# Kernel optimization log

Hardware: AMD Instinct MI355X
Metric: run time of the kernel (lower is better)

The kernel has to match this reference:

```python
import jax, jax.numpy as jnp
import numpy as np

OBS_LEN = 8
PRED_LEN = 12
BATCH = 65536
EMB = 64
H = 64


def setup_inputs() -> dict:
    key = jax.random.key(0)
    ks = jax.random.split(key, 18)
    s = 1.0 / np.sqrt(H)  # torch default uniform bound scale, used as std here

    def p(k, shape):
        return (jax.random.normal(k, shape, dtype=jnp.float32) * s).astype(jnp.float32)

    return {
        "obs_traj": jax.random.normal(ks[0], (OBS_LEN, BATCH, 2), dtype=jnp.float32),
        "obs_traj_rel": jax.random.normal(ks[1], (OBS_LEN, BATCH, 2), dtype=jnp.float32),
        # encoder params
        "enc_emb_w": p(ks[2], (EMB, 2)),
        "enc_emb_b": p(ks[3], (EMB,)),
        "enc_w_ih": p(ks[4], (4 * H, EMB)),
        "enc_w_hh": p(ks[5], (4 * H, H)),
        "enc_b_ih": p(ks[6], (4 * H,)),
        "enc_b_hh": p(ks[7], (4 * H,)),
        # decoder params
        "dec_emb_w": p(ks[8], (EMB, 2)),
        "dec_emb_b": p(ks[9], (EMB,)),
        "dec_w_ih": p(ks[10], (4 * H, EMB)),
        "dec_w_hh": p(ks[11], (4 * H, H)),
        "dec_b_ih": p(ks[12], (4 * H,)),
        "dec_b_hh": p(ks[13], (4 * H,)),
        "h2p_w": p(ks[14], (2, H)),
        "h2p_b": p(ks[15], (2,)),
    }


def _lstm_cell(h, c, x, w_ih, w_hh, b_ih, b_hh):
    # torch nn.LSTM gate order: i, f, g, o
    gates = x @ w_ih.T + h @ w_hh.T + (b_ih + b_hh)
    i, f, g, o = jnp.split(gates, 4, axis=-1)
    c_new = jax.nn.sigmoid(f) * c + jax.nn.sigmoid(i) * jnp.tanh(g)
    h_new = jax.nn.sigmoid(o) * jnp.tanh(c_new)
    return h_new, c_new


def reference(obs_traj, obs_traj_rel,
              enc_emb_w, enc_emb_b, enc_w_ih, enc_w_hh, enc_b_ih, enc_b_hh,
              dec_emb_w, dec_emb_b, dec_w_ih, dec_w_hh, dec_b_ih, dec_b_hh,
              h2p_w, h2p_b):
    batch = obs_traj_rel.shape[1]

    # ---------- Encoder ----------
    enc_in = obs_traj_rel @ enc_emb_w.T + enc_emb_b  # [T, B, EMB]

    def enc_step(carry, x_t):
        h, c = carry
        h, c = _lstm_cell(h, c, x_t, enc_w_ih, enc_w_hh, enc_b_ih, enc_b_hh)
        return (h, c), None

    h0 = jnp.zeros((batch, H), dtype=obs_traj_rel.dtype)
    c0 = jnp.zeros((batch, H), dtype=obs_traj_rel.dtype)
    (h_enc, _), _ = jax.lax.scan(enc_step, (h0, c0), enc_in)

    # ---------- Decoder ----------
    dec_h = h_enc                                   # final encoder hidden seeds decoder
    dec_c = jnp.zeros((batch, H), dtype=obs_traj_rel.dtype)
    last_pos_rel = obs_traj_rel[-1]
    dec_in = last_pos_rel @ dec_emb_w.T + dec_emb_b  # [B, EMB]

    def dec_step(carry, _):
        h, c, x = carry
        h, c = _lstm_cell(h, c, x, dec_w_ih, dec_w_hh, dec_b_ih, dec_b_hh)
        rel_pos = h @ h2p_w.T + h2p_b               # [B, 2]
        x_next = rel_pos @ dec_emb_w.T + dec_emb_b  # [B, EMB]
        return (h, c, x_next), rel_pos

    (_, _, _), pred_traj_fake_rel = jax.lax.scan(
        dec_step, (dec_h, dec_c, dec_in), None, length=PRED_LEN)
    return pred_traj_fake_rel  # [PRED_LEN, B, 2]
```

## Files before the change

kernel.cpp:

```cpp
#include <hip/hip_runtime.h>

#define OBS_LEN 8
#define PRED_LEN 12
#define TILE_B 32
#define NTHREADS 256

typedef __attribute__((ext_vector_type(8))) short short8;
typedef __attribute__((ext_vector_type(4))) float floatx4;
typedef __attribute__((ext_vector_type(2))) float floatx2;
typedef __attribute__((ext_vector_type(2))) unsigned int u32x2;
typedef unsigned short u16;
typedef unsigned int u32;

#define L2E 1.442695040888963f

__device__ __forceinline__ u16 f2bf(float f) {
  __bf16 b = (__bf16)f;
  return __builtin_bit_cast(u16, b);
}
__device__ __forceinline__ float bf2f(u16 h) {
  return __builtin_bit_cast(float, ((u32)h) << 16);
}
__device__ __forceinline__ float rndbf(float f) { return (float)(__bf16)f; }

#if __has_builtin(__builtin_amdgcn_exp2f)
__device__ __forceinline__ float fexp2_(float x) { return __builtin_amdgcn_exp2f(x); }
#else
__device__ __forceinline__ float fexp2_(float x) { return exp2f(x); }
#endif
__device__ __forceinline__ floatx2 exp2v(floatx2 x) {
  floatx2 r;
  r.x = fexp2_(x.x);
  r.y = fexp2_(x.y);
  return r;
}
#if __has_builtin(__builtin_amdgcn_rcpf)
__device__ __forceinline__ floatx2 rcp2(floatx2 x) {
  floatx2 r;
  r.x = __builtin_amdgcn_rcpf(x.x);
  r.y = __builtin_amdgcn_rcpf(x.y);
  return r;
}
#else
__device__ __forceinline__ floatx2 rcp2(floatx2 x) {
  return floatx2{1.0f / x.x, 1.0f / x.y};
}
#endif

__device__ __forceinline__ floatx4 mfma_bf(short8 a, short8 b, floatx4 c) {
  return __builtin_amdgcn_mfma_f32_16x16x32_bf16(a, b, c, 0, 0, 0);
}

__device__ __forceinline__ int swz(int s, int b) {
  return s * 64 + ((b ^ (s & 7)) * 8);
}

__device__ __forceinline__ void load_afrags(const float* __restrict__ W,
                                            short8 (&af)[4][2],
                                            int u0, int q, int l16) {
#pragma unroll
  for (int t = 0; t < 4; ++t)
#pragma unroll
    for (int kf = 0; kf < 2; ++kf) {
      const float* src = W + (t * 64 + u0 + l16) * 64 + kf * 32 + q * 8;
      const floatx4 w0 = *(const floatx4*)src;
      const floatx4 w1 = *(const floatx4*)(src + 4);
      short8 a;
#pragma unroll
      for (int j = 0; j < 4; ++j) {
        a[j] = (short)f2bf(w0[j]);
        a[j + 4] = (short)f2bf(w1[j]);
      }
      af[t][kf] = a;
    }
}

__device__ __forceinline__ void load_afrags_eff(const float* __restrict__ Whh,
                                                const float* __restrict__ aS0,
                                                const float* __restrict__ aS1,
                                                const float* __restrict__ hw0,
                                                const float* __restrict__ hw1,
                                                short8 (&af)[4][2],
                                                int u0, int q, int l16) {
#pragma unroll
  for (int t = 0; t < 4; ++t) {
    const int g = t * 64 + u0 + l16;
    const float a0 = aS0[g], a1 = aS1[g];
#pragma unroll
    for (int kf = 0; kf < 2; ++kf) {
      const int u = kf * 32 + q * 8;
      const float* src = Whh + g * 64 + u;
      const floatx4 w0 = *(const floatx4*)src;
      const floatx4 w1 = *(const floatx4*)(src + 4);
      const floatx4 p00 = *(const floatx4*)(hw0 + u);
      const floatx4 p01 = *(const floatx4*)(hw0 + u + 4);
      const floatx4 p10 = *(const floatx4*)(hw1 + u);
      const floatx4 p11 = *(const floatx4*)(hw1 + u + 4);
      short8 a;
#pragma unroll
      for (int j = 0; j < 4; ++j) {
        a[j] = (short)f2bf(w0[j] + a0 * p00[j] + a1 * p10[j]);
        a[j + 4] = (short)f2bf(w1[j] + a0 * p01[j] + a1 * p11[j]);
      }
      af[t][kf] = a;
    }
  }
}

__device__ __forceinline__ void nonlin_store(const floatx4 (&acc)[4],
                                             floatx2 (&c2)[2],
                                             u16* __restrict__ wrh,
                                             int s, int q, int wv) {
  const int sw = s & 7;
  u32 hpk[2];
#pragma unroll
  for (int p = 0; p < 2; ++p) {
    const floatx2 iv = {acc[0][2 * p], acc[0][2 * p + 1]};
    const floatx2 fv = {acc[1][2 * p], acc[1][2 * p + 1]};
    const floatx2 gv = {acc[2][2 * p], acc[2][2 * p + 1]};
    const floatx2 ov = {acc[3][2 * p], acc[3][2 * p + 1]};
    const floatx2 ei = exp2v(iv * -L2E);
    const floatx2 ef = exp2v(fv * -L2E);
    const floatx2 eg = exp2v(gv * (2.0f * L2E));
    const floatx2 eo = exp2v(ov * -L2E);
    const floatx2 A = ei + 1.0f;
    const floatx2 F = ef + 1.0f;
    const floatx2 Bg = eg + 1.0f;
    const floatx2 P = A * Bg;
    const floatx2 num = c2[p] * P + (eg - 1.0f) * F;
    const floatx2 cn = num * rcp2(F * P);
    c2[p] = cn;
    const floatx2 ec = exp2v(cn * (2.0f * L2E));
    const floatx2 h = (ec - 1.0f) * rcp2((eo + 1.0f) * (ec + 1.0f));
    hpk[p] = (u32)f2bf(h.x) | ((u32)f2bf(h.y) << 16);
  }
  *(u32x2*)(wrh + s * 64 + (((wv * 2 + (q >> 1)) ^ sw) * 8) + (q & 1) * 4) =
      u32x2{hpk[0], hpk[1]};
}

__device__ __forceinline__ void cell_step(const u16* __restrict__ rdh,
                                          const u16* __restrict__ rdx,
                                          u16* __restrict__ wrh,
                                          const short8 (&afh)[4][2],
                                          const short8 (&afx)[4][2],
                                          const float* __restrict__ biasrow,
                                          floatx2 (&c)[2][2],
                                          int q, int l16, int wv, int u0) {
#pragma unroll
  for (int n = 0; n < 2; ++n) {
    const int s = n * 16 + l16;
    const int sw = s & 7;
    const u16* hr = rdh + s * 64;
    const u16* xr = rdx + s * 64;
    const short8 hb0 = *(const short8*)(hr + ((q ^ sw) * 8));
    const short8 hb1 = *(const short8*)(hr + (((q + 4) ^ sw) * 8));
    const short8 xb0 = *(const short8*)(xr + ((q ^ sw) * 8));
    const short8 xb1 = *(const short8*)(xr + (((q + 4) ^ sw) * 8));
    floatx4 acc[4];
#pragma unroll
    for (int t = 0; t < 4; ++t) {
      const floatx4 bias = *(const floatx4*)(biasrow + t * 64 + u0 + q * 4);
      acc[t] = mfma_bf(afh[t][0], hb0, bias);
    }
#pragma unroll
    for (int t = 0; t < 4; ++t) acc[t] = mfma_bf(afx[t][0], xb0, acc[t]);
#pragma unroll
    for (int t = 0; t < 4; ++t) acc[t] = mfma_bf(afh[t][1], hb1, acc[t]);
#pragma unroll
    for (int t = 0; t < 4; ++t) acc[t] = mfma_bf(afx[t][1], xb1, acc[t]);
    nonlin_store(acc, c[n], wrh, s, q, wv);
  }
}

__device__ __forceinline__ void dec_step_folded(
    const u16* __restrict__ rdh, u16* __restrict__ wrh,
    const short8 (&af)[4][2], const short8 (&afp)[2],
    const float* __restrict__ biasrow, float b2p0, float b2p1,
    float* __restrict__ relrow,
    floatx2 (&c)[2][2], int q, int l16, int wv, int u0) {
  short8 hb0[2], hb1[2];
#pragma unroll
  for (int n = 0; n < 2; ++n) {
    const int s = n * 16 + l16, sw = s & 7;
    const u16* hr = rdh + s * 64;
    hb0[n] = *(const short8*)(hr + ((q ^ sw) * 8));
    hb1[n] = *(const short8*)(hr + (((q + 4) ^ sw) * 8));
  }
  floatx4 acc[2][4];
#pragma unroll
  for (int t = 0; t < 4; ++t) {
    const floatx4 bias = *(const floatx4*)(biasrow + t * 64 + u0 + q * 4);
    acc[0][t] = mfma_bf(af[t][0], hb0[0], bias);
    acc[1][t] = mfma_bf(af[t][0], hb0[1], bias);
  }
#pragma unroll
  for (int t = 0; t < 4; ++t) {
    acc[0][t] = mfma_bf(af[t][1], hb1[0], acc[0][t]);
    acc[1][t] = mfma_bf(af[t][1], hb1[1], acc[1][t]);
  }
  if (wv < 2) {
    const short8 ha = wv ? hb0[1] : hb0[0];
    const short8 hc = wv ? hb1[1] : hb1[0];
    floatx4 ar = mfma_bf(afp[0], ha, floatx4{0.f, 0.f, 0.f, 0.f});
    ar = mfma_bf(afp[1], hc, ar);
    if (q == 0)
      *(floatx2*)(relrow + (wv * 16 + l16) * 2) =
          floatx2{ar[0] + b2p0, ar[1] + b2p1};
  }
#pragma unroll
  for (int n = 0; n < 2; ++n)
    nonlin_store(acc[n], c[n], wrh, n * 16 + l16, q, wv);
}

__device__ __forceinline__ void xgen8(float rb0, float rb1,
                                      const float* __restrict__ ew0,
                                      const float* __restrict__ ew1,
                                      const float* __restrict__ eb,
                                      u16* __restrict__ xw, int s8, int p8) {
  short8 v;
#pragma unroll
  for (int j = 0; j < 8; ++j) {
    const int e = p8 * 8 + j;
    v[j] = (short)f2bf(rb0 * ew0[e] + (rb1 * ew1[e] + eb[e]));
  }
  *(short8*)(xw + swz(s8, p8)) = v;
}

__global__ void __launch_bounds__(NTHREADS, 3)
lstm_kernel(const float* __restrict__ obs_rel,
            const float* __restrict__ enc_emb_w, const float* __restrict__ enc_emb_b,
            const float* __restrict__ enc_w_ih, const float* __restrict__ enc_w_hh,
            const float* __restrict__ enc_b_ih, const float* __restrict__ enc_b_hh,
            const float* __restrict__ dec_emb_w, const float* __restrict__ dec_emb_b,
            const float* __restrict__ dec_w_ih, const float* __restrict__ dec_w_hh,
            const float* __restrict__ dec_b_ih, const float* __restrict__ dec_b_hh,
            const float* __restrict__ h2p_w, const float* __restrict__ h2p_b,
            float* __restrict__ out, int batch) {
  __shared__ __align__(16) u16 hS[2][TILE_B * 64];
  __shared__ __align__(16) u16 xS[2][TILE_B * 64];
  __shared__ __align__(16) float posS[OBS_LEN][TILE_B * 2];
  __shared__ __align__(16) float biasS[3][256];
  __shared__ float ew0e[64], ew1e[64], ebe[64];
  __shared__ float ew0d[64], ew1d[64], ebd[64];
  __shared__ __align__(16) float aS0[256], aS1[256];
  __shared__ __align__(16) float hw0S[64], hw1S[64];
  __shared__ __align__(16) float relS[PRED_LEN][TILE_B * 2];

  const int tid = threadIdx.x;
  const int wv = tid >> 6, lane = tid & 63;
  const int q = lane >> 4, l16 = lane & 15;
  const int u0 = wv << 4;
  const int s8 = tid >> 3, p8 = tid & 7;
  const long S0 = (long)blockIdx.x * TILE_B;

  if (tid < 128) {
    const int t = tid >> 4, i = tid & 15;
    *(floatx4*)&posS[t][i * 4] =
        *(const floatx4*)(obs_rel + (long)t * batch * 2 + S0 * 2 + i * 4);
  }
  if (tid < 64) {
    ew0e[tid] = rndbf(enc_emb_w[tid * 2]);
    ew1e[tid] = rndbf(enc_emb_w[tid * 2 + 1]);
    ebe[tid] = enc_emb_b[tid];
    ew0d[tid] = rndbf(dec_emb_w[tid * 2]);
    ew1d[tid] = rndbf(dec_emb_w[tid * 2 + 1]);
    ebd[tid] = dec_emb_b[tid];
    hw0S[tid] = h2p_w[tid];
    hw1S[tid] = h2p_w[64 + tid];
  }
  biasS[0][tid] = enc_b_ih[tid] + enc_b_hh[tid];
  {
    float A0 = 0.f, A1 = 0.f, B0 = 0.f;
    const float* wr = dec_w_ih + tid * 64;
#pragma unroll
    for (int e4 = 0; e4 < 16; ++e4) {
      const floatx4 w = *(const floatx4*)(wr + e4 * 4);
      const floatx4 m0 = *(const floatx4*)(dec_emb_w + e4 * 8);
      const floatx4 m1 = *(const floatx4*)(dec_emb_w + e4 * 8 + 4);
      const floatx4 bb = *(const floatx4*)(dec_emb_b + e4 * 4);
      A0 += w[0] * m0[0] + w[1] * m0[2] + w[2] * m1[0] + w[3] * m1[2];
      A1 += w[0] * m0[1] + w[1] * m0[3] + w[2] * m1[1] + w[3] * m1[3];
      B0 += w[0] * bb[0] + w[1] * bb[1] + w[2] * bb[2] + w[3] * bb[3];
    }
    aS0[tid] = A0;
    aS1[tid] = A1;
    const float db = dec_b_ih[tid] + dec_b_hh[tid];
    biasS[1][tid] = db;
    biasS[2][tid] = db + B0 + A0 * h2p_b[0] + A1 * h2p_b[1];
  }
  for (int i = tid; i < TILE_B * 64 / 2; i += NTHREADS) ((u32*)&hS[0][0])[i] = 0;

  short8 afh[4][2], afx[4][2];
  floatx2 c[2][2];
  load_afrags(enc_w_hh, afh, u0, q, l16);
  load_afrags(enc_w_ih, afx, u0, q, l16);
  c[0][0] = c[0][1] = c[1][0] = c[1][1] = floatx2{0.f, 0.f};
  const float b2p0 = h2p_b[0], b2p1 = h2p_b[1];
  __syncthreads();
  {
    const floatx2 rr = *(const floatx2*)(&posS[0][s8 * 2]);
    xgen8(rndbf(rr.x), rndbf(rr.y), ew0e, ew1e, ebe, xS[0], s8, p8);
  }
  __syncthreads();

  int pb = 0;
#pragma unroll 1
  for (int t = 0; t < OBS_LEN; ++t) {
    const int tn = t + 1;
    const floatx2 rr = *(const floatx2*)(&posS[(tn < 8) ? tn : 7][s8 * 2]);
    if (tn < 8)
      xgen8(rndbf(rr.x), rndbf(rr.y), ew0e, ew1e, ebe, xS[tn & 1], s8, p8);
    else
      xgen8(rndbf(rr.x), rndbf(rr.y), ew0d, ew1d, ebd, xS[0], s8, p8);
    cell_step(hS[pb], xS[t & 1], hS[pb ^ 1], afh, afx, &biasS[0][0], c,
              q, l16, wv, u0);
    __syncthreads();
    pb ^= 1;
  }

  load_afrags(dec_w_hh, afh, u0, q, l16);
  load_afrags(dec_w_ih, afx, u0, q, l16);
  c[0][0] = c[0][1] = c[1][0] = c[1][1] = floatx2{0.f, 0.f};
  cell_step(hS[pb], xS[0], hS[pb ^ 1], afh, afx, &biasS[1][0], c,
            q, l16, wv, u0);
  load_afrags_eff(dec_w_hh, aS0, aS1, hw0S, hw1S, afh, u0, q, l16);
  short8 afp[2];
#pragma unroll
  for (int kf = 0; kf < 2; ++kf) {
    const int kb = kf * 32 + q * 8;
    short8 a;
#pragma unroll
    for (int j = 0; j < 4; ++j) {
      const float r0 = (l16 == 0) ? hw0S[kb + j] : (l16 == 1) ? hw1S[kb + j] : 0.f;
      const float r1 =
          (l16 == 0) ? hw0S[kb + 4 + j] : (l16 == 1) ? hw1S[kb + 4 + j] : 0.f;
      a[j] = (short)f2bf(r0);
      a[j + 4] = (short)f2bf(r1);
    }
    afp[kf] = a;
  }
  __syncthreads();
  pb ^= 1;

#pragma unroll 1
  for (int j = 1; j < PRED_LEN; ++j) {
    dec_step_folded(hS[pb], hS[pb ^ 1], afh, afp, &biasS[2][0], b2p0, b2p1,
                    &relS[j - 1][0], c, q, l16, wv, u0);
    __syncthreads();
    pb ^= 1;
  }

  if (wv < 2) {
    const int s = wv * 16 + l16, sw = s & 7;
    const u16* hr = hS[pb] + s * 64;
    const short8 ha = *(const short8*)(hr + ((q ^ sw) * 8));
    const short8 hc = *(const short8*)(hr + (((q + 4) ^ sw) * 8));
    floatx4 ar = mfma_bf(afp[0], ha, floatx4{0.f, 0.f, 0.f, 0.f});
    ar = mfma_bf(afp[1], hc, ar);
    if (q == 0)
      *(floatx2*)(&relS[PRED_LEN - 1][s * 2]) =
          floatx2{ar[0] + b2p0, ar[1] + b2p1};
  }
  __syncthreads();

#pragma unroll
  for (int r = 0; r < 3; ++r) {
    const int f = tid + r * 256;
    const int j = f >> 6, e = f & 63;
    out[(long)j * batch * 2 + S0 * 2 + e] = ((const float*)relS)[f];
  }
}

extern "C" void kernel_launch(void* const* d_in, const int* in_sizes, int n_in,
                              void* d_out, int out_size, void* d_ws, size_t ws_size,
                              hipStream_t stream) {
  const float* obs_rel = (const float*)d_in[1];
  const int batch = in_sizes[1] / (OBS_LEN * 2);

  const int blocks = batch / TILE_B;
  hipLaunchKernelGGL(lstm_kernel, dim3(blocks), dim3(NTHREADS), 0, stream,
                     obs_rel,
                     (const float*)d_in[2], (const float*)d_in[3],
                     (const float*)d_in[4], (const float*)d_in[5],
                     (const float*)d_in[6], (const float*)d_in[7],
                     (const float*)d_in[8], (const float*)d_in[9],
                     (const float*)d_in[10], (const float*)d_in[11],
                     (const float*)d_in[12], (const float*)d_in[13],
                     (const float*)d_in[14], (const float*)d_in[15],
                     (float*)d_out, batch);
}
```

Baseline: 218.5 us.

## Fold encoder input embedding into rank-2 gate weights, drop x tiles

Folds the embedding linear layer into the input-to-hidden weights, giving a rank-2 matrix per gate row plus a folded bias, for both encoder and first decoder step. The per-step input contribution becomes one MFMA against a mostly-zero fragment holding the two raw positions, replacing two MFMAs on a 64-wide embedded x. This removes the xS shared buffers and the per-step xgen work. The decoder rel-pos MFMA is moved inside the per-n loop to cut live registers, and launch bounds rise from 3 to 4 blocks per CU. Rounding changes slightly, because positions and folded weights are now cast to bf16 directly instead of the embedded activations.

```diff
diff --git a/kernel.cpp b/kernel.cpp
--- a/kernel.cpp
+++ b/kernel.cpp
@@ -51,10 +51,6 @@
   return __builtin_amdgcn_mfma_f32_16x16x32_bf16(a, b, c, 0, 0, 0);
 }
 
-__device__ __forceinline__ int swz(int s, int b) {
-  return s * 64 + ((b ^ (s & 7)) * 8);
-}
-
 __device__ __forceinline__ void load_afrags(const float* __restrict__ W,
                                             short8 (&af)[4][2],
                                             int u0, int q, int l16) {
@@ -104,6 +100,39 @@
       }
       af[t][kf] = a;
     }
+  }
+}
+
+__device__ __forceinline__ void fold_rank2(const float* __restrict__ wr,
+                                           const float* __restrict__ emb_w,
+                                           const float* __restrict__ emb_b,
+                                           float& A0, float& A1, float& B0) {
+  A0 = A1 = B0 = 0.f;
+#pragma unroll
+  for (int e4 = 0; e4 < 16; ++e4) {
+    const floatx4 w = *(const floatx4*)(wr + e4 * 4);
+    const floatx4 m0 = *(const floatx4*)(emb_w + e4 * 8);
+    const floatx4 m1 = *(const floatx4*)(emb_w + e4 * 8 + 4);
+    const floatx4 bb = *(const floatx4*)(emb_b + e4 * 4);
+    A0 += w[0] * m0[0] + w[1] * m0[2] + w[2] * m1[0] + w[3] * m1[2];
+    A1 += w[0] * m0[1] + w[1] * m0[3] + w[2] * m1[1] + w[3] * m1[3];
+    B0 += w[0] * bb[0] + w[1] * bb[1] + w[2] * bb[2] + w[3] * bb[3];
+  }
+}
+
+__device__ __forceinline__ void build_gfrag(const float* __restrict__ A0t,
+                                            const float* __restrict__ A1t,
+                                            short8 (&gf)[4],
+                                            int u0, int q, int l16) {
+#pragma unroll
+  for (int t = 0; t < 4; ++t) {
+    short8 a = short8{0, 0, 0, 0, 0, 0, 0, 0};
+    if (q == 0) {
+      const int g = t * 64 + u0 + l16;
+      a[0] = (short)f2bf(A0t[g]);
+      a[1] = (short)f2bf(A1t[g]);
+    }
+    gf[t] = a;
   }
 }
 
@@ -138,36 +167,33 @@
       u32x2{hpk[0], hpk[1]};
 }
 
-__device__ __forceinline__ void cell_step(const u16* __restrict__ rdh,
-                                          const u16* __restrict__ rdx,
-                                          u16* __restrict__ wrh,
-                                          const short8 (&afh)[4][2],
-                                          const short8 (&afx)[4][2],
-                                          const float* __restrict__ biasrow,
-                                          floatx2 (&c)[2][2],
-                                          int q, int l16, int wv, int u0) {
+__device__ __forceinline__ void cell_step_fold(
+    const u16* __restrict__ rdh, u16* __restrict__ wrh,
+    const short8 (&afh)[4][2], const short8 (&gf)[4],
+    const float* __restrict__ biasrow, const float* __restrict__ posrow,
+    floatx2 (&c)[2][2], int q, int l16, int wv, int u0) {
 #pragma unroll
   for (int n = 0; n < 2; ++n) {
-    const int s = n * 16 + l16;
-    const int sw = s & 7;
+    const int s = n * 16 + l16, sw = s & 7;
     const u16* hr = rdh + s * 64;
-    const u16* xr = rdx + s * 64;
     const short8 hb0 = *(const short8*)(hr + ((q ^ sw) * 8));
     const short8 hb1 = *(const short8*)(hr + (((q + 4) ^ sw) * 8));
-    const short8 xb0 = *(const short8*)(xr + ((q ^ sw) * 8));
-    const short8 xb1 = *(const short8*)(xr + (((q + 4) ^ sw) * 8));
+    const floatx2 pp = *(const floatx2*)(posrow + s * 2);
+    short8 pf = short8{0, 0, 0, 0, 0, 0, 0, 0};
+    if (q == 0) {
+      pf[0] = (short)f2bf(pp.x);
+      pf[1] = (short)f2bf(pp.y);
+    }
     floatx4 acc[4];
 #pragma unroll
     for (int t = 0; t < 4; ++t) {
       const floatx4 bias = *(const floatx4*)(biasrow + t * 64 + u0 + q * 4);
-      acc[t] = mfma_bf(afh[t][0], hb0, bias);
-    }
-#pragma unroll
-    for (int t = 0; t < 4; ++t) acc[t] = mfma_bf(afx[t][0], xb0, acc[t]);
+      acc[t] = mfma_bf(gf[t], pf, bias);
+    }
+#pragma unroll
+    for (int t = 0; t < 4; ++t) acc[t] = mfma_bf(afh[t][0], hb0, acc[t]);
 #pragma unroll
     for (int t = 0; t < 4; ++t) acc[t] = mfma_bf(afh[t][1], hb1, acc[t]);
-#pragma unroll
-    for (int t = 0; t < 4; ++t) acc[t] = mfma_bf(afx[t][1], xb1, acc[t]);
     nonlin_store(acc, c[n], wrh, s, q, wv);
   }
 }
@@ -178,55 +204,31 @@
     const float* __restrict__ biasrow, float b2p0, float b2p1,
     float* __restrict__ relrow,
     floatx2 (&c)[2][2], int q, int l16, int wv, int u0) {
-  short8 hb0[2], hb1[2];
 #pragma unroll
   for (int n = 0; n < 2; ++n) {
     const int s = n * 16 + l16, sw = s & 7;
     const u16* hr = rdh + s * 64;
-    hb0[n] = *(const short8*)(hr + ((q ^ sw) * 8));
-    hb1[n] = *(const short8*)(hr + (((q + 4) ^ sw) * 8));
-  }
-  floatx4 acc[2][4];
-#pragma unroll
-  for (int t = 0; t < 4; ++t) {
-    const floatx4 bias = *(const floatx4*)(biasrow + t * 64 + u0 + q * 4);
-    acc[0][t] = mfma_bf(af[t][0], hb0[0], bias);
-    acc[1][t] = mfma_bf(af[t][0], hb0[1], bias);
-  }
-#pragma unroll
-  for (int t = 0; t < 4; ++t) {
-    acc[0][t] = mfma_bf(af[t][1], hb1[0], acc[0][t]);
-    acc[1][t] = mfma_bf(af[t][1], hb1[1], acc[1][t]);
-  }
-  if (wv < 2) {
-    const short8 ha = wv ? hb0[1] : hb0[0];
-    const short8 hc = wv ? hb1[1] : hb1[0];
-    floatx4 ar = mfma_bf(afp[0], ha, floatx4{0.f, 0.f, 0.f, 0.f});
-    ar = mfma_bf(afp[1], hc, ar);
-    if (q == 0)
-      *(floatx2*)(relrow + (wv * 16 + l16) * 2) =
-          floatx2{ar[0] + b2p0, ar[1] + b2p1};
-  }
-#pragma unroll
-  for (int n = 0; n < 2; ++n)
-    nonlin_store(acc[n], c[n], wrh, n * 16 + l16, q, wv);
-}
-
-__device__ __forceinline__ void xgen8(float rb0, float rb1,
-                                      const float* __restrict__ ew0,
-                                      const float* __restrict__ ew1,
-                                      const float* __restrict__ eb,
-                                      u16* __restrict__ xw, int s8, int p8) {
-  short8 v;
-#pragma unroll
-  for (int j = 0; j < 8; ++j) {
-    const int e = p8 * 8 + j;
-    v[j] = (short)f2bf(rb0 * ew0[e] + (rb1 * ew1[e] + eb[e]));
-  }
-  *(short8*)(xw + swz(s8, p8)) = v;
-}
-
-__global__ void __launch_bounds__(NTHREADS, 3)
+    const short8 hb0 = *(const short8*)(hr + ((q ^ sw) * 8));
+    const short8 hb1 = *(const short8*)(hr + (((q + 4) ^ sw) * 8));
+    floatx4 acc[4];
+#pragma unroll
+    for (int t = 0; t < 4; ++t) {
+      const floatx4 bias = *(const floatx4*)(biasrow + t * 64 + u0 + q * 4);
+      acc[t] = mfma_bf(af[t][0], hb0, bias);
+    }
+#pragma unroll
+    for (int t = 0; t < 4; ++t) acc[t] = mfma_bf(af[t][1], hb1, acc[t]);
+    if (wv == n) {
+      floatx4 ar = mfma_bf(afp[0], hb0, floatx4{0.f, 0.f, 0.f, 0.f});
+      ar = mfma_bf(afp[1], hb1, ar);
+      if (q == 0)
+        *(floatx2*)(relrow + s * 2) = floatx2{ar[0] + b2p0, ar[1] + b2p1};
+    }
+    nonlin_store(acc, c[n], wrh, s, q, wv);
+  }
+}
+
+__global__ void __launch_bounds__(NTHREADS, 4)
 lstm_kernel(const float* __restrict__ obs_rel,
             const float* __restrict__ enc_emb_w, const float* __restrict__ enc_emb_b,
             const float* __restrict__ enc_w_ih, const float* __restrict__ enc_w_hh,
@@ -237,12 +239,10 @@
             const float* __restrict__ h2p_w, const float* __restrict__ h2p_b,
             float* __restrict__ out, int batch) {
   __shared__ __align__(16) u16 hS[2][TILE_B * 64];
-  __shared__ __align__(16) u16 xS[2][TILE_B * 64];
   __shared__ __align__(16) float posS[OBS_LEN][TILE_B * 2];
   __shared__ __align__(16) float biasS[3][256];
-  __shared__ float ew0e[64], ew1e[64], ebe[64];
-  __shared__ float ew0d[64], ew1d[64], ebd[64];
-  __shared__ __align__(16) float aS0[256], aS1[256];
+  __shared__ __align__(16) float eA0[256], eA1[256];
+  __shared__ __align__(16) float dA0[256], dA1[256];
   __shared__ __align__(16) float hw0S[64], hw1S[64];
   __shared__ __align__(16) float relS[PRED_LEN][TILE_B * 2];
 
@@ -250,7 +250,6 @@
   const int wv = tid >> 6, lane = tid & 63;
   const int q = lane >> 4, l16 = lane & 15;
   const int u0 = wv << 4;
-  const int s8 = tid >> 3, p8 = tid & 7;
   const long S0 = (long)blockIdx.x * TILE_B;
 
   if (tid < 128) {
@@ -259,71 +258,47 @@
         *(const floatx4*)(obs_rel + (long)t * batch * 2 + S0 * 2 + i * 4);
   }
   if (tid < 64) {
-    ew0e[tid] = rndbf(enc_emb_w[tid * 2]);
-    ew1e[tid] = rndbf(enc_emb_w[tid * 2 + 1]);
-    ebe[tid] = enc_emb_b[tid];
-    ew0d[tid] = rndbf(dec_emb_w[tid * 2]);
-    ew1d[tid] = rndbf(dec_emb_w[tid * 2 + 1]);
-    ebd[tid] = dec_emb_b[tid];
     hw0S[tid] = h2p_w[tid];
     hw1S[tid] = h2p_w[64 + tid];
   }
-  biasS[0][tid] = enc_b_ih[tid] + enc_b_hh[tid];
   {
-    float A0 = 0.f, A1 = 0.f, B0 = 0.f;
-    const float* wr = dec_w_ih + tid * 64;
-#pragma unroll
-    for (int e4 = 0; e4 < 16; ++e4) {
-      const floatx4 w = *(const floatx4*)(wr + e4 * 4);
-      const floatx4 m0 = *(const floatx4*)(dec_emb_w + e4 * 8);
-      const floatx4 m1 = *(const floatx4*)(dec_emb_w + e4 * 8 + 4);
-      const floatx4 bb = *(const floatx4*)(dec_emb_b + e4 * 4);
-      A0 += w[0] * m0[0] + w[1] * m0[2] + w[2] * m1[0] + w[3] * m1[2];
-      A1 += w[0] * m0[1] + w[1] * m0[3] + w[2] * m1[1] + w[3] * m1[3];
-      B0 += w[0] * bb[0] + w[1] * bb[1] + w[2] * bb[2] + w[3] * bb[3];
-    }
-    aS0[tid] = A0;
-    aS1[tid] = A1;
-    const float db = dec_b_ih[tid] + dec_b_hh[tid];
+    float A0, A1, B0;
+    fold_rank2(enc_w_ih + tid * 64, enc_emb_w, enc_emb_b, A0, A1, B0);
+    eA0[tid] = A0;
+    eA1[tid] = A1;
+    biasS[0][tid] = enc_b_ih[tid] + enc_b_hh[tid] + B0;
+    fold_rank2(dec_w_ih + tid * 64, dec_emb_w, dec_emb_b, A0, A1, B0);
+    dA0[tid] = A0;
+    dA1[tid] = A1;
+    const float db = dec_b_ih[tid] + dec_b_hh[tid] + B0;
     biasS[1][tid] = db;
-    biasS[2][tid] = db + B0 + A0 * h2p_b[0] + A1 * h2p_b[1];
+    biasS[2][tid] = db + A0 * h2p_b[0] + A1 * h2p_b[1];
   }
   for (int i = tid; i < TILE_B * 64 / 2; i += NTHREADS) ((u32*)&hS[0][0])[i] = 0;
 
-  short8 afh[4][2], afx[4][2];
+  short8 afh[4][2], gf[4];
   floatx2 c[2][2];
   load_afrags(enc_w_hh, afh, u0, q, l16);
-  load_afrags(enc_w_ih, afx, u0, q, l16);
   c[0][0] = c[0][1] = c[1][0] = c[1][1] = floatx2{0.f, 0.f};
   const float b2p0 = h2p_b[0], b2p1 = h2p_b[1];
   __syncthreads();
-  {
-    const floatx2 rr = *(const floatx2*)(&posS[0][s8 * 2]);
-    xgen8(rndbf(rr.x), rndbf(rr.y), ew0e, ew1e, ebe, xS[0], s8, p8);
-  }
-  __syncthreads();
+  build_gfrag(eA0, eA1, gf, u0, q, l16);
 
   int pb = 0;
 #pragma unroll 1
   for (int t = 0; t < OBS_LEN; ++t) {
-    const int tn = t + 1;
-    const floatx2 rr = *(const floatx2*)(&posS[(tn < 8) ? tn : 7][s8 * 2]);
-    if (tn < 8)
-      xgen8(rndbf(rr.x), rndbf(rr.y), ew0e, ew1e, ebe, xS[tn & 1], s8, p8);
-    else
-      xgen8(rndbf(rr.x), rndbf(rr.y), ew0d, ew1d, ebd, xS[0], s8, p8);
-    cell_step(hS[pb], xS[t & 1], hS[pb ^ 1], afh, afx, &biasS[0][0], c,
-              q, l16, wv, u0);
+    cell_step_fold(hS[pb], hS[pb ^ 1], afh, gf, &biasS[0][0], &posS[t][0], c,
+                   q, l16, wv, u0);
     __syncthreads();
     pb ^= 1;
   }
 
   load_afrags(dec_w_hh, afh, u0, q, l16);
-  load_afrags(dec_w_ih, afx, u0, q, l16);
+  build_gfrag(dA0, dA1, gf, u0, q, l16);
   c[0][0] = c[0][1] = c[1][0] = c[1][1] = floatx2{0.f, 0.f};
-  cell_step(hS[pb], xS[0], hS[pb ^ 1], afh, afx, &biasS[1][0], c,
-            q, l16, wv, u0);
-  load_afrags_eff(dec_w_hh, aS0, aS1, hw0S, hw1S, afh, u0, q, l16);
+  cell_step_fold(hS[pb], hS[pb ^ 1], afh, gf, &biasS[1][0], &posS[7][0], c,
+                 q, l16, wv, u0);
+  load_afrags_eff(dec_w_hh, dA0, dA1, hw0S, hw1S, afh, u0, q, l16);
   short8 afp[2];
 #pragma unroll
   for (int kf = 0; kf < 2; ++kf) {
```

Measured after the change: 214.0 us. -2.1%, faster.
